# Performance work log

Hardware: AMD Instinct MI355X
Metric: run time of the kernel (lower is better)

The kernel has to match this reference:

```python
import jax, jax.numpy as jnp
import jax.scipy.linalg as jsl
import numpy as np

B, C_IN, T = 32, 64, 256
Z = 32
HID = [256, 256]
K = 3


def conv1d_same(x, W, b):
    # x: (B, C_in, T), W: (C_out, C_in, K) -> (B, C_out, T)
    y = jax.lax.conv_general_dilated(x, W, window_strides=(1,), padding='SAME',
                                     dimension_numbers=('NCH', 'OIH', 'NCH'))
    return y + b[None, :, None]


def setup_inputs() -> dict:
    key = jax.random.key(0)
    ks = jax.random.split(key, 4)
    scale = lambda fan_in: 1.0 / np.sqrt(fan_in)
    x = jax.random.normal(ks[0], (B, C_IN, T), dtype=jnp.float32)
    W0 = jax.random.normal(ks[1], (HID[0], C_IN, K), dtype=jnp.float32) * scale(C_IN * K)
    b0 = jnp.zeros((HID[0],), jnp.float32)
    W1 = jax.random.normal(ks[2], (HID[1], HID[0], K), dtype=jnp.float32) * scale(HID[0] * K)
    b1 = jnp.zeros((HID[1],), jnp.float32)
    W2 = jax.random.normal(ks[3], (3 * Z, HID[1], K), dtype=jnp.float32) * scale(HID[1] * K)
    b2 = jnp.zeros((3 * Z,), jnp.float32)
    return {"x": x, "W0": W0, "b0": b0, "W1": W1, "b1": b1, "W2": W2, "b2": b2}


def reference(x, W0, b0, W1, b1, W2, b2):
    batch, seq_len = x.shape[0], x.shape[-1]
    h = jax.nn.relu(conv1d_same(x, W0, b0))
    h = jax.nn.relu(conv1d_same(h, W1, b1))
    stats = conv1d_same(h, W2, b2)                       # (B, 3z, T)
    z = stats.shape[1] // 3
    mu = stats[:, :z]                                    # (B, z, T)
    prec = jax.nn.softplus(stats[:, z:])                 # (B, 2z, T), precision_activation
    # torch: reshape (B, 2z, T) -> (B, z, 2T), drop last value -> 2T-1 params per (b, z)
    prec = prec.reshape(batch, z, 2 * seq_len)[..., :-1]
    diag = prec[..., :seq_len]                           # (B, z, T)  diagonal entries
    sup = prec[..., seq_len:]                            # (B, z, T-1) superdiagonal entries
    # build upper-bidiagonal precision P = I + diag + superdiag
    i = jnp.arange(seq_len)
    j = jnp.arange(seq_len - 1)
    P = jnp.zeros((batch, z, seq_len, seq_len), dtype=x.dtype)
    P = P.at[..., i, i].set(diag + 1.0)
    P = P.at[..., j, j + 1].set(sup)
    eye = jnp.broadcast_to(jnp.eye(seq_len, dtype=x.dtype), P.shape)
    # covariance upper-triangular factor: solve P @ U = I (P upper triangular)
    cov_u = jsl.solve_triangular(P, eye, lower=False)
    cov_u = jnp.where(jnp.isfinite(cov_u), cov_u, jnp.zeros_like(cov_u))
    scale_tril = jnp.swapaxes(cov_u, -1, -2)             # lower triangular (B, z, T, T)
    return mu, scale_tril
```

## Files before the change

kernel.cpp:

```cpp
#include <hip/hip_runtime.h>
#include <hip/hip_bf16.h>
#include <math.h>

#define BB 32
#define TT 256
#define ZDIM 32

typedef float vf4 __attribute__((ext_vector_type(4)));
typedef short short8 __attribute__((ext_vector_type(8)));
typedef short short4v __attribute__((ext_vector_type(4)));
typedef float f32x4 __attribute__((ext_vector_type(4)));

__device__ __forceinline__ float softplus_f(float v) {
    return fmaxf(v, 0.0f) + log1pf(expf(-fabsf(v)));
}

__device__ __forceinline__ unsigned short f2bf(float f) {
    __hip_bfloat16 h = __float2bfloat16(f);
    return *reinterpret_cast<unsigned short*>(&h);
}

template<int COUT, int CIN>
__device__ void wconv_frag(const float* __restrict__ W, unsigned short* __restrict__ Wb,
                           int tid, int nthreads)
{
    const int n = 3 * COUT * CIN;
    for (int idx = tid; idx < n; idx += nthreads) {
        int j     = idx & 7;
        int lane  = (idx >> 3) & 63;
        int rest  = idx >> 9;
        int kch   = rest % (CIN / 32);
        int rest2 = rest / (CIN / 32);
        int ot    = rest2 % (COUT / 16);
        int ks    = rest2 / (COUT / 16);
        int o  = ot * 16 + (lane & 15);
        int ci = kch * 32 + (lane >> 4) * 8 + j;
        Wb[idx] = f2bf(W[(o * CIN + ci) * 3 + ks]);
    }
}

__global__ __launch_bounds__(256)
void wconv_kernel(const float* __restrict__ W0, const float* __restrict__ W1,
                  const float* __restrict__ W2, unsigned short* __restrict__ w0b,
                  unsigned short* __restrict__ w1b, unsigned short* __restrict__ w2b)
{
    const int tid = blockIdx.x * blockDim.x + threadIdx.x;
    const int nth = gridDim.x * blockDim.x;
    wconv_frag<256, 64>(W0, w0b, tid, nth);
    wconv_frag<256, 256>(W1, w1b, tid, nth);
    wconv_frag<96, 256>(W2, w2b, tid, nth);
}

__global__ __launch_bounds__(1024, 1)
void fused_conv(const float* __restrict__ x,
                const unsigned short* __restrict__ w0b,
                const unsigned short* __restrict__ w1b,
                const unsigned short* __restrict__ w2b,
                const float* __restrict__ b0, const float* __restrict__ b1,
                const float* __restrict__ b2,
                float* __restrict__ mu, float* __restrict__ dd,
                float* __restrict__ ss)
{
    constexpr int XPAD = 72;
    constexpr int HPAD = 264;

    __shared__ __attribute__((aligned(16))) unsigned short xsb[64][XPAD];
    __shared__ __attribute__((aligned(16))) unsigned short h0s[48][HPAD];
    __shared__ __attribute__((aligned(16))) unsigned short h1s[34][HPAD];

    const int b    = blockIdx.x;
    const int t0   = blockIdx.y * 32;
    const int tid  = threadIdx.x;
    const int wv   = tid >> 6;
    const int lane = tid & 63;
    const int l15  = lane & 15;
    const int quad = lane >> 4;

    if (wv < 8) {
        const int ci = lane;
        const int t8 = t0 - 16 + wv * 8;
        unsigned short v[8];
        if (t8 >= 0 && t8 < TT) {
            const float* xp = x + (size_t)(b * 64 + ci) * TT + t8;
            f32x4 lo = *(const f32x4*)xp;
            f32x4 hi = *(const f32x4*)(xp + 4);
            #pragma unroll
            for (int j = 0; j < 4; ++j) { v[j] = f2bf(lo[j]); v[4 + j] = f2bf(hi[j]); }
        } else {
            #pragma unroll
            for (int j = 0; j < 8; ++j) v[j] = 0;
        }
        #pragma unroll
        for (int j = 0; j < 8; ++j) xsb[wv * 8 + j][ci] = v[j];
    }
    __syncthreads();

    {
        f32x4 a1[3];
        {
            f32x4 bv;
            #pragma unroll
            for (int r = 0; r < 4; ++r) bv[r] = b0[wv * 16 + quad * 4 + r];
            #pragma unroll
            for (int nt = 0; nt < 3; ++nt) a1[nt] = bv;
        }
        #pragma unroll
        for (int ks = 0; ks < 3; ++ks) {
            #pragma unroll
            for (int kc = 0; kc < 64; kc += 32) {
                short8 af = *(const short8*)(w0b + (size_t)((ks * 16 + wv) * 2 + (kc >> 5)) * 512 + lane * 8);
                #pragma unroll
                for (int nt = 0; nt < 3; ++nt) {
                    short8 bf = *(const short8*)&xsb[nt * 16 + l15 + ks + 7][kc + quad * 8];
                    a1[nt] = __builtin_amdgcn_mfma_f32_16x16x32_bf16(af, bf, a1[nt], 0, 0, 0);
                }
            }
        }
        #pragma unroll
        for (int nt = 0; nt < 3; ++nt) {
            int p = nt * 16 + l15;
            int t = t0 - 8 + p;
            bool ok = (t >= 0) && (t < TT);
            short4v v;
            #pragma unroll
            for (int r = 0; r < 4; ++r)
                v[r] = ok ? (short)f2bf(fmaxf(a1[nt][r], 0.f)) : (short)0;
            *(short4v*)&h0s[p][wv * 16 + quad * 4] = v;
        }
    }
    __syncthreads();

    {
        f32x4 a2[3];
        {
            f32x4 bv;
            #pragma unroll
            for (int r = 0; r < 4; ++r) bv[r] = b1[wv * 16 + quad * 4 + r];
            #pragma unroll
            for (int nt = 0; nt < 3; ++nt) a2[nt] = bv;
        }
        #pragma unroll 1
        for (int c0 = 0; c0 < 256; c0 += 64) {
            #pragma unroll
            for (int ks = 0; ks < 3; ++ks) {
                #pragma unroll
                for (int kc = 0; kc < 64; kc += 32) {
                    short8 af = *(const short8*)(w1b + (size_t)((ks * 16 + wv) * 8 + ((c0 + kc) >> 5)) * 512 + lane * 8);
                    #pragma unroll
                    for (int nt = 0; nt < 3; ++nt) {
                        constexpr int F2[3] = {6, 22, 24};
                        short8 bf = *(const short8*)&h0s[F2[nt] + l15 + ks][c0 + kc + quad * 8];
                        a2[nt] = __builtin_amdgcn_mfma_f32_16x16x32_bf16(af, bf, a2[nt], 0, 0, 0);
                    }
                }
            }
        }
        #pragma unroll
        for (int nt = 0; nt < 3; ++nt) {
            constexpr int P2[3]  = {0, 16, 18};
            constexpr int TO2[3] = {-1, 15, 17};
            int p = P2[nt] + l15;
            int t = t0 + TO2[nt] + l15;
            bool ok = (t >= 0) && (t < TT);
            short4v v;
            #pragma unroll
            for (int r = 0; r < 4; ++r)
                v[r] = ok ? (short)f2bf(fmaxf(a2[nt][r], 0.f)) : (short)0;
            *(short4v*)&h1s[p][wv * 16 + quad * 4] = v;
        }
    }
    __syncthreads();

    if (wv < 12) {
        const int ot = wv % 6;
        const int nt = wv / 6;
        f32x4 a3;
        #pragma unroll
        for (int r = 0; r < 4; ++r) a3[r] = b2[ot * 16 + quad * 4 + r];
        #pragma unroll 1
        for (int c0 = 0; c0 < 256; c0 += 64) {
            #pragma unroll
            for (int ks = 0; ks < 3; ++ks) {
                #pragma unroll
                for (int kc = 0; kc < 64; kc += 32) {
                    short8 af = *(const short8*)(w2b + (size_t)((ks * 6 + ot) * 8 + ((c0 + kc) >> 5)) * 512 + lane * 8);
                    short8 bf = *(const short8*)&h1s[nt * 16 + l15 + ks][c0 + kc + quad * 8];
                    a3 = __builtin_amdgcn_mfma_f32_16x16x32_bf16(af, bf, a3, 0, 0, 0);
                }
            }
        }
        const int t = t0 + nt * 16 + l15;
        #pragma unroll
        for (int r = 0; r < 4; ++r) {
            int o = ot * 16 + quad * 4 + r;
            float val = a3[r];
            if (o < ZDIM) {
                mu[(b * ZDIM + o) * TT + t] = val;
            } else {
                int oc = o - ZDIM;
                int z  = oc >> 1;
                float sp = softplus_f(val);
                if ((oc & 1) == 0) dd[(b * ZDIM + z) * TT + t] = sp + 1.f;
                else               ss[(b * ZDIM + z) * TT + t] = sp;
            }
        }
    }
}

__global__ __launch_bounds__(256)
void tril_kernel(const float* __restrict__ dd, const float* __restrict__ ss,
                 float* __restrict__ out)
{
    __shared__ float invd[TT];
    __shared__ float tt[TT];

    const int bz  = blockIdx.x;
    const int tid = threadIdx.x;

    {
        float d  = dd[bz * TT + tid];
        float s  = ss[bz * TT + tid];
        float iv = 1.0f / d;
        invd[tid] = iv;
        tt[tid]   = -s * iv;
    }
    __syncthreads();

    const int r0 = (tid >> 6) * 64;
    const int c0 = (tid & 63) * 4;

    float p0 = 1.f, p1 = 1.f, p2 = 1.f, p3 = 1.f;
    for (int k = 0; k < r0 - 1; ++k) {
        float tm = tt[k];
        p0 = (k >= c0    ) ? p0 * tm : p0;
        p1 = (k >= c0 + 1) ? p1 * tm : p1;
        p2 = (k >= c0 + 2) ? p2 * tm : p2;
        p3 = (k >= c0 + 3) ? p3 * tm : p3;
    }
    p0 = (c0     < r0) ? p0 : 0.f;
    p1 = (c0 + 1 < r0) ? p1 : 0.f;
    p2 = (c0 + 2 < r0) ? p2 : 0.f;
    p3 = (c0 + 3 < r0) ? p3 : 0.f;

    float* orow = out + (size_t)bz * TT * TT + (size_t)r0 * TT + c0;

    #pragma unroll 2
    for (int r = r0; r < r0 + 64; ++r) {
        float tm = (r > 0) ? tt[r - 1] : 0.0f;
        p0 = (r == c0    ) ? 1.0f : p0 * tm;
        p1 = (r == c0 + 1) ? 1.0f : p1 * tm;
        p2 = (r == c0 + 2) ? 1.0f : p2 * tm;
        p3 = (r == c0 + 3) ? 1.0f : p3 * tm;
        float id = invd[r];
        vf4 v;
        v.x = p0 * id; v.y = p1 * id; v.z = p2 * id; v.w = p3 * id;
        v.x = isfinite(v.x) ? v.x : 0.0f;
        v.y = isfinite(v.y) ? v.y : 0.0f;
        v.z = isfinite(v.z) ? v.z : 0.0f;
        v.w = isfinite(v.w) ? v.w : 0.0f;
        __builtin_nontemporal_store(v, (vf4*)orow);
        orow += TT;
    }
}

extern "C" void kernel_launch(void* const* d_in, const int* in_sizes, int n_in,
                              void* d_out, int out_size, void* d_ws, size_t ws_size,
                              hipStream_t stream)
{
    const float* x  = (const float*)d_in[0];
    const float* W0 = (const float*)d_in[1];
    const float* b0 = (const float*)d_in[2];
    const float* W1 = (const float*)d_in[3];
    const float* b1 = (const float*)d_in[4];
    const float* W2 = (const float*)d_in[5];
    const float* b2 = (const float*)d_in[6];

    float* out = (float*)d_out;
    float* mu  = out;
    float* st  = out + BB * ZDIM * TT;

    float* dd = (float*)d_ws;
    float* ss = dd + BB * ZDIM * TT;
    unsigned short* w0b = (unsigned short*)(ss + BB * ZDIM * TT);
    unsigned short* w1b = w0b + 3 * 256 * 64;
    unsigned short* w2b = w1b + 3 * 256 * 256;

    wconv_kernel<<<dim3(256), 256, 0, stream>>>(W0, W1, W2, w0b, w1b, w2b);
    fused_conv<<<dim3(BB, 8), 1024, 0, stream>>>(
        x, w0b, w1b, w2b, b0, b1, b2, mu, dd, ss);
    tril_kernel<<<dim3(BB * ZDIM), 256, 0, stream>>>(dd, ss, st);
}
```

Measured before the change: 300.0 us.

## Merge three kernels into one cooperative kernel with grid-wide syncs

Replaces the weight-conversion, fused conv, and tril kernels with a single cooperative mega-kernel of 256 blocks of 1024 threads. The phases are separated by grid.sync, and the tril phase reuses the shared memory through a union. The goal is to remove two kernel launch gaps and the inter-kernel drain/fill. The cost is that the tril phase now runs on 256 large blocks instead of 1024 small ones, so occupancy is lower, and each grid barrier carries its own overhead.

```diff
diff --git a/kernel.cpp b/kernel.cpp
--- a/kernel.cpp
+++ b/kernel.cpp
@@ -1,6 +1,9 @@
 #include <hip/hip_runtime.h>
+#include <hip/hip_cooperative_groups.h>
 #include <hip/hip_bf16.h>
 #include <math.h>
+
+namespace cg = cooperative_groups;
 
 #define BB 32
 #define TT 256
@@ -39,227 +42,239 @@
     }
 }
 
-__global__ __launch_bounds__(256)
-void wconv_kernel(const float* __restrict__ W0, const float* __restrict__ W1,
-                  const float* __restrict__ W2, unsigned short* __restrict__ w0b,
-                  unsigned short* __restrict__ w1b, unsigned short* __restrict__ w2b)
+__global__ __launch_bounds__(1024, 1)
+void mega_kernel(const float* __restrict__ x,
+                 const float* __restrict__ W0, const float* __restrict__ b0,
+                 const float* __restrict__ W1, const float* __restrict__ b1,
+                 const float* __restrict__ W2, const float* __restrict__ b2,
+                 float* __restrict__ mu, float* __restrict__ dd,
+                 float* __restrict__ ss, float* __restrict__ st,
+                 unsigned short* __restrict__ w0b,
+                 unsigned short* __restrict__ w1b,
+                 unsigned short* __restrict__ w2b)
 {
-    const int tid = blockIdx.x * blockDim.x + threadIdx.x;
-    const int nth = gridDim.x * blockDim.x;
-    wconv_frag<256, 64>(W0, w0b, tid, nth);
-    wconv_frag<256, 256>(W1, w1b, tid, nth);
-    wconv_frag<96, 256>(W2, w2b, tid, nth);
-}
-
-__global__ __launch_bounds__(1024, 1)
-void fused_conv(const float* __restrict__ x,
-                const unsigned short* __restrict__ w0b,
-                const unsigned short* __restrict__ w1b,
-                const unsigned short* __restrict__ w2b,
-                const float* __restrict__ b0, const float* __restrict__ b1,
-                const float* __restrict__ b2,
-                float* __restrict__ mu, float* __restrict__ dd,
-                float* __restrict__ ss)
-{
-    constexpr int XPAD = 72;
-    constexpr int HPAD = 264;
-
-    __shared__ __attribute__((aligned(16))) unsigned short xsb[64][XPAD];
-    __shared__ __attribute__((aligned(16))) unsigned short h0s[48][HPAD];
-    __shared__ __attribute__((aligned(16))) unsigned short h1s[34][HPAD];
-
-    const int b    = blockIdx.x;
-    const int t0   = blockIdx.y * 32;
+    cg::grid_group grid = cg::this_grid();
+
+    __shared__ __attribute__((aligned(16))) union {
+        struct {
+            unsigned short xsb[64][72];
+            unsigned short h0s[48][264];
+            unsigned short h1s[34][264];
+        } c;
+        struct {
+            float invd[4][TT];
+            float tt[4][TT];
+        } t;
+    } sm;
+
     const int tid  = threadIdx.x;
     const int wv   = tid >> 6;
     const int lane = tid & 63;
     const int l15  = lane & 15;
     const int quad = lane >> 4;
 
-    if (wv < 8) {
-        const int ci = lane;
-        const int t8 = t0 - 16 + wv * 8;
-        unsigned short v[8];
-        if (t8 >= 0 && t8 < TT) {
-            const float* xp = x + (size_t)(b * 64 + ci) * TT + t8;
-            f32x4 lo = *(const f32x4*)xp;
-            f32x4 hi = *(const f32x4*)(xp + 4);
-            #pragma unroll
-            for (int j = 0; j < 4; ++j) { v[j] = f2bf(lo[j]); v[4 + j] = f2bf(hi[j]); }
-        } else {
-            #pragma unroll
-            for (int j = 0; j < 8; ++j) v[j] = 0;
-        }
-        #pragma unroll
-        for (int j = 0; j < 8; ++j) xsb[wv * 8 + j][ci] = v[j];
+    {
+        const int gtid = blockIdx.x * blockDim.x + tid;
+        const int nth  = gridDim.x * blockDim.x;
+        wconv_frag<256, 64>(W0, w0b, gtid, nth);
+        wconv_frag<256, 256>(W1, w1b, gtid, nth);
+        wconv_frag<96, 256>(W2, w2b, gtid, nth);
     }
-    __syncthreads();
+    __threadfence();
+    grid.sync();
 
     {
-        f32x4 a1[3];
+        const int b  = blockIdx.x >> 3;
+        const int t0 = (blockIdx.x & 7) * 32;
+        auto& xsb = sm.c.xsb;
+        auto& h0s = sm.c.h0s;
+        auto& h1s = sm.c.h1s;
+
+        if (wv < 8) {
+            const int ci = lane;
+            const int t8 = t0 - 16 + wv * 8;
+            unsigned short v[8];
+            if (t8 >= 0 && t8 < TT) {
+                const float* xp = x + (size_t)(b * 64 + ci) * TT + t8;
+                f32x4 lo = *(const f32x4*)xp;
+                f32x4 hi = *(const f32x4*)(xp + 4);
+                #pragma unroll
+                for (int j = 0; j < 4; ++j) { v[j] = f2bf(lo[j]); v[4 + j] = f2bf(hi[j]); }
+            } else {
+                #pragma unroll
+                for (int j = 0; j < 8; ++j) v[j] = 0;
+            }
+            #pragma unroll
+            for (int j = 0; j < 8; ++j) xsb[wv * 8 + j][ci] = v[j];
+        }
+        __syncthreads();
+
         {
-            f32x4 bv;
-            #pragma unroll
-            for (int r = 0; r < 4; ++r) bv[r] = b0[wv * 16 + quad * 4 + r];
-            #pragma unroll
-            for (int nt = 0; nt < 3; ++nt) a1[nt] = bv;
-        }
-        #pragma unroll
-        for (int ks = 0; ks < 3; ++ks) {
-            #pragma unroll
-            for (int kc = 0; kc < 64; kc += 32) {
-                short8 af = *(const short8*)(w0b + (size_t)((ks * 16 + wv) * 2 + (kc >> 5)) * 512 + lane * 8);
-                #pragma unroll
-                for (int nt = 0; nt < 3; ++nt) {
-                    short8 bf = *(const short8*)&xsb[nt * 16 + l15 + ks + 7][kc + quad * 8];
-                    a1[nt] = __builtin_amdgcn_mfma_f32_16x16x32_bf16(af, bf, a1[nt], 0, 0, 0);
-                }
-            }
-        }
-        #pragma unroll
-        for (int nt = 0; nt < 3; ++nt) {
-            int p = nt * 16 + l15;
-            int t = t0 - 8 + p;
-            bool ok = (t >= 0) && (t < TT);
-            short4v v;
-            #pragma unroll
-            for (int r = 0; r < 4; ++r)
-                v[r] = ok ? (short)f2bf(fmaxf(a1[nt][r], 0.f)) : (short)0;
-            *(short4v*)&h0s[p][wv * 16 + quad * 4] = v;
-        }
-    }
-    __syncthreads();
-
-    {
-        f32x4 a2[3];
-        {
-            f32x4 bv;
-            #pragma unroll
-            for (int r = 0; r < 4; ++r) bv[r] = b1[wv * 16 + quad * 4 + r];
-            #pragma unroll
-            for (int nt = 0; nt < 3; ++nt) a2[nt] = bv;
-        }
-        #pragma unroll 1
-        for (int c0 = 0; c0 < 256; c0 += 64) {
+            f32x4 a1[3];
+            {
+                f32x4 bv;
+                #pragma unroll
+                for (int r = 0; r < 4; ++r) bv[r] = b0[wv * 16 + quad * 4 + r];
+                #pragma unroll
+                for (int nt = 0; nt < 3; ++nt) a1[nt] = bv;
+            }
             #pragma unroll
             for (int ks = 0; ks < 3; ++ks) {
                 #pragma unroll
                 for (int kc = 0; kc < 64; kc += 32) {
-                    short8 af = *(const short8*)(w1b + (size_t)((ks * 16 + wv) * 8 + ((c0 + kc) >> 5)) * 512 + lane * 8);
+                    short8 af = *(const short8*)(w0b + (size_t)((ks * 16 + wv) * 2 + (kc >> 5)) * 512 + lane * 8);
                     #pragma unroll
                     for (int nt = 0; nt < 3; ++nt) {
-                        constexpr int F2[3] = {6, 22, 24};
-                        short8 bf = *(const short8*)&h0s[F2[nt] + l15 + ks][c0 + kc + quad * 8];
-                        a2[nt] = __builtin_amdgcn_mfma_f32_16x16x32_bf16(af, bf, a2[nt], 0, 0, 0);
+                        short8 bf = *(const short8*)&xsb[nt * 16 + l15 + ks + 7][kc + quad * 8];
+                        a1[nt] = __builtin_amdgcn_mfma_f32_16x16x32_bf16(af, bf, a1[nt], 0, 0, 0);
                     }
                 }
             }
-        }
-        #pragma unroll
-        for (int nt = 0; nt < 3; ++nt) {
-            constexpr int P2[3]  = {0, 16, 18};
-            constexpr int TO2[3] = {-1, 15, 17};
-            int p = P2[nt] + l15;
-            int t = t0 + TO2[nt] + l15;
-            bool ok = (t >= 0) && (t < TT);
-            short4v v;
-            #pragma unroll
-            for (int r = 0; r < 4; ++r)
-                v[r] = ok ? (short)f2bf(fmaxf(a2[nt][r], 0.f)) : (short)0;
-            *(short4v*)&h1s[p][wv * 16 + quad * 4] = v;
+            #pragma unroll
+            for (int nt = 0; nt < 3; ++nt) {
+                int p = nt * 16 + l15;
+                int t = t0 - 8 + p;
+                bool ok = (t >= 0) && (t < TT);
+                short4v v;
+                #pragma unroll
+                for (int r = 0; r < 4; ++r)
+                    v[r] = ok ? (short)f2bf(fmaxf(a1[nt][r], 0.f)) : (short)0;
+                *(short4v*)&h0s[p][wv * 16 + quad * 4] = v;
+            }
+        }
+        __syncthreads();
+
+        {
+            f32x4 a2[3];
+            {
+                f32x4 bv;
+                #pragma unroll
+                for (int r = 0; r < 4; ++r) bv[r] = b1[wv * 16 + quad * 4 + r];
+                #pragma unroll
+                for (int nt = 0; nt < 3; ++nt) a2[nt] = bv;
+            }
+            #pragma unroll 1
+            for (int c0 = 0; c0 < 256; c0 += 64) {
+                #pragma unroll
+                for (int ks = 0; ks < 3; ++ks) {
+                    #pragma unroll
+                    for (int kc = 0; kc < 64; kc += 32) {
+                        short8 af = *(const short8*)(w1b + (size_t)((ks * 16 + wv) * 8 + ((c0 + kc) >> 5)) * 512 + lane * 8);
+                        #pragma unroll
+                        for (int nt = 0; nt < 3; ++nt) {
+                            constexpr int F2[3] = {6, 22, 24};
+                            short8 bf = *(const short8*)&h0s[F2[nt] + l15 + ks][c0 + kc + quad * 8];
+                            a2[nt] = __builtin_amdgcn_mfma_f32_16x16x32_bf16(af, bf, a2[nt], 0, 0, 0);
+                        }
+                    }
+                }
+            }
+            #pragma unroll
+            for (int nt = 0; nt < 3; ++nt) {
+                constexpr int P2[3]  = {0, 16, 18};
+                constexpr int TO2[3] = {-1, 15, 17};
+                int p = P2[nt] + l15;
+                int t = t0 + TO2[nt] + l15;
+                bool ok = (t >= 0) && (t < TT);
+                short4v v;
+                #pragma unroll
+                for (int r = 0; r < 4; ++r)
+                    v[r] = ok ? (short)f2bf(fmaxf(a2[nt][r], 0.f)) : (short)0;
+                *(short4v*)&h1s[p][wv * 16 + quad * 4] = v;
+            }
+        }
+        __syncthreads();
+
+        if (wv < 12) {
+            const int ot = wv % 6;
+            const int nt = wv / 6;
+            f32x4 a3;
+            #pragma unroll
+            for (int r = 0; r < 4; ++r) a3[r] = b2[ot * 16 + quad * 4 + r];
+            #pragma unroll 1
+            for (int c0 = 0; c0 < 256; c0 += 64) {
+                #pragma unroll
+                for (int ks = 0; ks < 3; ++ks) {
+                    #pragma unroll
+                    for (int kc = 0; kc < 64; kc += 32) {
+                        short8 af = *(const short8*)(w2b + (size_t)((ks * 6 + ot) * 8 + ((c0 + kc) >> 5)) * 512 + lane * 8);
+                        short8 bf = *(const short8*)&h1s[nt * 16 + l15 + ks][c0 + kc + quad * 8];
+                        a3 = __builtin_amdgcn_mfma_f32_16x16x32_bf16(af, bf, a3, 0, 0, 0);
+                    }
+                }
+            }
+            const int t = t0 + nt * 16 + l15;
+            #pragma unroll
+            for (int r = 0; r < 4; ++r) {
+                int o = ot * 16 + quad * 4 + r;
+                float val = a3[r];
+                if (o < ZDIM) {
+                    mu[(b * ZDIM + o) * TT + t] = val;
+                } else {
+                    int oc = o - ZDIM;
+                    int z  = oc >> 1;
+                    float sp = softplus_f(val);
+                    if ((oc & 1) == 0) dd[(b * ZDIM + z) * TT + t] = sp + 1.f;
+                    else               ss[(b * ZDIM + z) * TT + t] = sp;
+                }
+            }
         }
     }
-    __syncthreads();
-
-    if (wv < 12) {
-        const int ot = wv % 6;
-        const int nt = wv / 6;
-        f32x4 a3;
-        #pragma unroll
-        for (int r = 0; r < 4; ++r) a3[r] = b2[ot * 16 + quad * 4 + r];
-        #pragma unroll 1
-        for (int c0 = 0; c0 < 256; c0 += 64) {
-            #pragma unroll
-            for (int ks = 0; ks < 3; ++ks) {
-                #pragma unroll
-                for (int kc = 0; kc < 64; kc += 32) {
-                    short8 af = *(const short8*)(w2b + (size_t)((ks * 6 + ot) * 8 + ((c0 + kc) >> 5)) * 512 + lane * 8);
-                    short8 bf = *(const short8*)&h1s[nt * 16 + l15 + ks][c0 + kc + quad * 8];
-                    a3 = __builtin_amdgcn_mfma_f32_16x16x32_bf16(af, bf, a3, 0, 0, 0);
-                }
-            }
-        }
-        const int t = t0 + nt * 16 + l15;
-        #pragma unroll
-        for (int r = 0; r < 4; ++r) {
-            int o = ot * 16 + quad * 4 + r;
-            float val = a3[r];
-            if (o < ZDIM) {
-                mu[(b * ZDIM + o) * TT + t] = val;
-            } else {
-                int oc = o - ZDIM;
-                int z  = oc >> 1;
-                float sp = softplus_f(val);
-                if ((oc & 1) == 0) dd[(b * ZDIM + z) * TT + t] = sp + 1.f;
-                else               ss[(b * ZDIM + z) * TT + t] = sp;
-            }
-        }
-    }
-}
-
-__global__ __launch_bounds__(256)
-void tril_kernel(const float* __restrict__ dd, const float* __restrict__ ss,
-                 float* __restrict__ out)
-{
-    __shared__ float invd[TT];
-    __shared__ float tt[TT];
-
-    const int bz  = blockIdx.x;
-    const int tid = threadIdx.x;
+    __threadfence();
+    grid.sync();
 
     {
-        float d  = dd[bz * TT + tid];
-        float s  = ss[bz * TT + tid];
-        float iv = 1.0f / d;
-        invd[tid] = iv;
-        tt[tid]   = -s * iv;
-    }
-    __syncthreads();
-
-    const int r0 = (tid >> 6) * 64;
-    const int c0 = (tid & 63) * 4;
-
-    float p0 = 1.f, p1 = 1.f, p2 = 1.f, p3 = 1.f;
-    for (int k = 0; k < r0 - 1; ++k) {
-        float tm = tt[k];
-        p0 = (k >= c0    ) ? p0 * tm : p0;
-        p1 = (k >= c0 + 1) ? p1 * tm : p1;
-        p2 = (k >= c0 + 2) ? p2 * tm : p2;
-        p3 = (k >= c0 + 3) ? p3 * tm : p3;
-    }
-    p0 = (c0     < r0) ? p0 : 0.f;
-    p1 = (c0 + 1 < r0) ? p1 : 0.f;
-    p2 = (c0 + 2 < r0) ? p2 : 0.f;
-    p3 = (c0 + 3 < r0) ? p3 : 0.f;
-
-    float* orow = out + (size_t)bz * TT * TT + (size_t)r0 * TT + c0;
-
-    #pragma unroll 2
-    for (int r = r0; r < r0 + 64; ++r) {
-        float tm = (r > 0) ? tt[r - 1] : 0.0f;
-        p0 = (r == c0    ) ? 1.0f : p0 * tm;
-        p1 = (r == c0 + 1) ? 1.0f : p1 * tm;
-        p2 = (r == c0 + 2) ? 1.0f : p2 * tm;
-        p3 = (r == c0 + 3) ? 1.0f : p3 * tm;
-        float id = invd[r];
-        vf4 v;
-        v.x = p0 * id; v.y = p1 * id; v.z = p2 * id; v.w = p3 * id;
-        v.x = isfinite(v.x) ? v.x : 0.0f;
-        v.y = isfinite(v.y) ? v.y : 0.0f;
-        v.z = isfinite(v.z) ? v.z : 0.0f;
-        v.w = isfinite(v.w) ? v.w : 0.0f;
-        __builtin_nontemporal_store(v, (vf4*)orow);
-        orow += TT;
+        const int g    = wv >> 2;
+        const int bz   = blockIdx.x * 4 + g;
+        const int w4   = wv & 3;
+        const int tloc = (w4 << 6) | lane;
+
+        {
+            float d  = dd[bz * TT + tloc];
+            float s  = ss[bz * TT + tloc];
+            float iv = 1.0f / d;
+            sm.t.invd[g][tloc] = iv;
+            sm.t.tt[g][tloc]   = -s * iv;
+        }
+        __syncthreads();
+
+        const float* invd = sm.t.invd[g];
+        const float* tt   = sm.t.tt[g];
+        const int r0 = w4 * 64;
+        const int c0 = lane * 4;
+
+        float p0 = 1.f, p1 = 1.f, p2 = 1.f, p3 = 1.f;
+        for (int k = 0; k < r0 - 1; ++k) {
+            float tm = tt[k];
+            p0 = (k >= c0    ) ? p0 * tm : p0;
+            p1 = (k >= c0 + 1) ? p1 * tm : p1;
+            p2 = (k >= c0 + 2) ? p2 * tm : p2;
+            p3 = (k >= c0 + 3) ? p3 * tm : p3;
+        }
+        p0 = (c0     < r0) ? p0 : 0.f;
+        p1 = (c0 + 1 < r0) ? p1 : 0.f;
+        p2 = (c0 + 2 < r0) ? p2 : 0.f;
+        p3 = (c0 + 3 < r0) ? p3 : 0.f;
+
+        float* orow = st + (size_t)bz * TT * TT + (size_t)r0 * TT + c0;
+
+        #pragma unroll 2
+        for (int r = r0; r < r0 + 64; ++r) {
+            float tm = (r > 0) ? tt[r - 1] : 0.0f;
+            p0 = (r == c0    ) ? 1.0f : p0 * tm;
+            p1 = (r == c0 + 1) ? 1.0f : p1 * tm;
+            p2 = (r == c0 + 2) ? 1.0f : p2 * tm;
+            p3 = (r == c0 + 3) ? 1.0f : p3 * tm;
+            float id = invd[r];
+            vf4 v;
+            v.x = p0 * id; v.y = p1 * id; v.z = p2 * id; v.w = p3 * id;
+            v.x = isfinite(v.x) ? v.x : 0.0f;
+            v.y = isfinite(v.y) ? v.y : 0.0f;
+            v.z = isfinite(v.z) ? v.z : 0.0f;
+            v.w = isfinite(v.w) ? v.w : 0.0f;
+            __builtin_nontemporal_store(v, (vf4*)orow);
+            orow += TT;
+        }
     }
 }
 
@@ -285,8 +300,11 @@
     unsigned short* w1b = w0b + 3 * 256 * 64;
     unsigned short* w2b = w1b + 3 * 256 * 256;
 
-    wconv_kernel<<<dim3(256), 256, 0, stream>>>(W0, W1, W2, w0b, w1b, w2b);
-    fused_conv<<<dim3(BB, 8), 1024, 0, stream>>>(
-        x, w0b, w1b, w2b, b0, b1, b2, mu, dd, ss);
-    tril_kernel<<<dim3(BB * ZDIM), 256, 0, stream>>>(dd, ss, st);
-}
+    void* args[] = {
+        (void*)&x, (void*)&W0, (void*)&b0, (void*)&W1, (void*)&b1,
+        (void*)&W2, (void*)&b2, (void*)&mu, (void*)&dd, (void*)&ss,
+        (void*)&st, (void*)&w0b, (void*)&w1b, (void*)&w2b
+    };
+    hipLaunchCooperativeKernel((void*)mega_kernel, dim3(BB * 8), dim3(1024),
+                               args, 0, stream);
+}
```

New measurement: 516.7 us. +72.3%, slower.
